# Performance work log

Hardware: AMD Instinct MI355X
Metric: run time of the kernel (lower is better)

The kernel has to match this reference:

```python
import jax, jax.numpy as jnp
import numpy as np

N_NODES = 50000
N_EDGES = 640000
D_IN = 128
D_OUT = 128


def setup_inputs() -> dict:
    key = jax.random.key(0)
    k1, k2, k3, k4, k5, k6 = jax.random.split(key, 6)
    nfeat = jax.random.normal(k1, (N_NODES, D_IN), dtype=jnp.float32)
    w = jax.random.uniform(k2, (N_EDGES,), dtype=jnp.float32)
    # nn.Linear weights are [out_feats, in_feats], Kaiming-uniform-ish scale
    bound = 1.0 / np.sqrt(D_IN)
    W1 = jax.random.uniform(k3, (D_OUT, D_IN), dtype=jnp.float32, minval=-bound, maxval=bound)
    W2 = jax.random.uniform(k4, (D_OUT, D_IN), dtype=jnp.float32, minval=-bound, maxval=bound)
    src = jax.random.randint(k5, (N_EDGES,), 0, N_NODES, dtype=jnp.int64)
    dst = jax.random.randint(k6, (N_EDGES,), 0, N_NODES, dtype=jnp.int64)
    return {"nfeat": nfeat, "w": w, "W1": W1, "W2": W2, "src": src, "dst": dst}


def reference(nfeat, w, W1, W2, src, dst):
    # feat_drop is identity in eval mode
    h = nfeat  # [N, D_IN]
    # update_all(u_mul_e('h','w','m'), sum('m','h_neighbor')):
    # gather source features, scale by per-edge scalar weight, scatter-sum to dst
    msg = h[src] * w[:, None]                                   # [E, D_IN]
    h_neighbor = jax.ops.segment_sum(msg, dst, num_segments=h.shape[0])  # [N, D_IN]
    # Bi-interaction residual: leaky_relu(Linear(h + hn)) + leaky_relu(Linear(h * hn))
    add_branch = jax.nn.leaky_relu((h + h_neighbor) @ W1.T, negative_slope=0.01)
    mul_branch = jax.nn.leaky_relu((h * h_neighbor) @ W2.T, negative_slope=0.01)
    out = add_branch + mul_branch                                # [N, D_OUT]
    return (h_neighbor, out)
```

## Files before the change

### kernel.cpp

```cpp
#include <hip/hip_runtime.h>
#include <hip/hip_bf16.h>

#define N_NODES 50000
#define N_EDGES 640000
#define D 128
#define OUT0_ELEMS (N_NODES * D)
#define SCAN_BLOCKS ((N_NODES + 255) / 256)

typedef __attribute__((ext_vector_type(8))) short short8v;
typedef __attribute__((ext_vector_type(4))) short short4v;
typedef __attribute__((ext_vector_type(4))) float f32x4;

static __device__ __forceinline__ unsigned short f2bf(float x) {
  __hip_bfloat16 b = __float2bfloat16(x);
  return *reinterpret_cast<unsigned short*>(&b);
}
static __device__ __forceinline__ float bf2f(unsigned short u) {
  unsigned x = ((unsigned)u) << 16;
  return __builtin_bit_cast(float, x);
}
static __device__ __forceinline__ unsigned pack_edge(int s, float wv) {
  return ((unsigned)f2bf(wv) << 16) | (unsigned)s;
}

__global__ __launch_bounds__(256) void conv_all(
    const float* __restrict__ nfeat, const float* __restrict__ W1,
    const float* __restrict__ W2, unsigned short* __restrict__ nf16,
    unsigned short* __restrict__ wc, int* __restrict__ cnt) {
  int i = blockIdx.x * 256 + threadIdx.x;
  int base = i * 8;
  float4 a = *(const float4*)(nfeat + base);
  float4 b = *(const float4*)(nfeat + base + 4);
  short8v o;
  o[0] = (short)f2bf(a.x); o[1] = (short)f2bf(a.y);
  o[2] = (short)f2bf(a.z); o[3] = (short)f2bf(a.w);
  o[4] = (short)f2bf(b.x); o[5] = (short)f2bf(b.y);
  o[6] = (short)f2bf(b.z); o[7] = (short)f2bf(b.w);
  *(short8v*)(nf16 + base) = o;
  if (i < D * D) {
    wc[i] = f2bf(W1[i]);
    wc[D * D + i] = f2bf(W2[i]);
  }
  if (i < N_NODES) cnt[i] = 0;
}

__global__ __launch_bounds__(256) void hist_rank(
    const int* __restrict__ dst, int* __restrict__ cnt, int* __restrict__ rank) {
  int t = blockIdx.x * 256 + threadIdx.x;
  int e = t * 4;
  if (e >= N_EDGES) return;
  int4 d4 = *(const int4*)(dst + e);
  int4 r4;
  r4.x = atomicAdd(&cnt[d4.x], 1);
  r4.y = atomicAdd(&cnt[d4.y], 1);
  r4.z = atomicAdd(&cnt[d4.z], 1);
  r4.w = atomicAdd(&cnt[d4.w], 1);
  *(int4*)(rank + e) = r4;
}

__global__ __launch_bounds__(256) void scan_block(
    const int* __restrict__ cnt, int* __restrict__ offs, int* __restrict__ bsums) {
  __shared__ int sdata[256];
  int t = threadIdx.x;
  int i = blockIdx.x * 256 + t;
  int v = (i < N_NODES) ? cnt[i] : 0;
  sdata[t] = v;
  __syncthreads();
#pragma unroll
  for (int off = 1; off < 256; off <<= 1) {
    int x = (t >= off) ? sdata[t - off] : 0;
    __syncthreads();
    sdata[t] += x;
    __syncthreads();
  }
  if (i < N_NODES) offs[i] = sdata[t] - v;
  if (t == 255) bsums[blockIdx.x] = sdata[t];
}

static __device__ __forceinline__ void scan_bsums_lds(
    const int* __restrict__ bsums, int* sincl) {
  int t = threadIdx.x;
  int v = (t < SCAN_BLOCKS) ? bsums[t] : 0;
  sincl[t] = v;
  __syncthreads();
#pragma unroll
  for (int off = 1; off < 256; off <<= 1) {
    int x = (t >= off) ? sincl[t - off] : 0;
    __syncthreads();
    sincl[t] += x;
    __syncthreads();
  }
}

__global__ __launch_bounds__(256) void fill4(
    const int* __restrict__ src, const int* __restrict__ dst,
    const float* __restrict__ w, const int* __restrict__ rank,
    const int* __restrict__ offs, const int* __restrict__ bsums,
    unsigned* __restrict__ es) {
  __shared__ int sincl[256];
  scan_bsums_lds(bsums, sincl);
  int t = blockIdx.x * 256 + threadIdx.x;
  int e = t * 4;
  if (e >= N_EDGES) return;
  int4 d4 = *(const int4*)(dst + e);
  int4 r4 = *(const int4*)(rank + e);
  int4 s4 = *(const int4*)(src + e);
  float4 w4 = *(const float4*)(w + e);
  int p0 = offs[d4.x] + ((d4.x >> 8) ? sincl[(d4.x >> 8) - 1] : 0) + r4.x;
  int p1 = offs[d4.y] + ((d4.y >> 8) ? sincl[(d4.y >> 8) - 1] : 0) + r4.y;
  int p2 = offs[d4.z] + ((d4.z >> 8) ? sincl[(d4.z >> 8) - 1] : 0) + r4.z;
  int p3 = offs[d4.w] + ((d4.w >> 8) ? sincl[(d4.w >> 8) - 1] : 0) + r4.w;
  es[p0] = pack_edge(s4.x, w4.x);
  es[p1] = pack_edge(s4.y, w4.y);
  es[p2] = pack_edge(s4.z, w4.z);
  es[p3] = pack_edge(s4.w, w4.w);
}

__global__ __launch_bounds__(256) void gather_bf16(
    const unsigned short* __restrict__ nf16, const int* __restrict__ offs,
    const int* __restrict__ bsums, const unsigned* __restrict__ es,
    float* __restrict__ hn) {
  __shared__ int sincl[256];
  scan_bsums_lds(bsums, sincl);

  int tid = blockIdx.x * 256 + threadIdx.x;
  int node = tid >> 4;
  if (node >= N_NODES) return;
  int q = tid & 15;

  int beg = offs[node] + ((node >> 8) ? sincl[(node >> 8) - 1] : 0);
  int end;
  {
    int n1 = node + 1;
    end = (n1 == N_NODES) ? N_EDGES
                          : offs[n1] + ((n1 >> 8) ? sincl[(n1 >> 8) - 1] : 0);
  }

  float acc[8];
#pragma unroll
  for (int j = 0; j < 8; ++j) acc[j] = 0.f;

  int k = beg;
  for (; k + 3 < end; k += 4) {
    unsigned r0 = es[k], r1 = es[k + 1], r2 = es[k + 2], r3 = es[k + 3];
    short8v v0 = *(const short8v*)(nf16 + (size_t)(r0 & 0xFFFF) * D + q * 8);
    short8v v1 = *(const short8v*)(nf16 + (size_t)(r1 & 0xFFFF) * D + q * 8);
    short8v v2 = *(const short8v*)(nf16 + (size_t)(r2 & 0xFFFF) * D + q * 8);
    short8v v3 = *(const short8v*)(nf16 + (size_t)(r3 & 0xFFFF) * D + q * 8);
    float w0 = bf2f((unsigned short)(r0 >> 16));
    float w1 = bf2f((unsigned short)(r1 >> 16));
    float w2 = bf2f((unsigned short)(r2 >> 16));
    float w3 = bf2f((unsigned short)(r3 >> 16));
#pragma unroll
    for (int j = 0; j < 8; ++j) {
      acc[j] += bf2f((unsigned short)v0[j]) * w0;
      acc[j] += bf2f((unsigned short)v1[j]) * w1;
      acc[j] += bf2f((unsigned short)v2[j]) * w2;
      acc[j] += bf2f((unsigned short)v3[j]) * w3;
    }
  }
  for (; k < end; ++k) {
    unsigned r0 = es[k];
    short8v v0 = *(const short8v*)(nf16 + (size_t)(r0 & 0xFFFF) * D + q * 8);
    float w0 = bf2f((unsigned short)(r0 >> 16));
#pragma unroll
    for (int j = 0; j < 8; ++j) acc[j] += bf2f((unsigned short)v0[j]) * w0;
  }

  float* orow = hn + (size_t)node * D + q * 8;
  *(float4*)(orow) = make_float4(acc[0], acc[1], acc[2], acc[3]);
  *(float4*)(orow + 4) = make_float4(acc[4], acc[5], acc[6], acc[7]);
}

__global__ __launch_bounds__(256) void bi_mfma_h16(
    const unsigned short* __restrict__ h16, const float* __restrict__ hn,
    const unsigned short* __restrict__ wc, float* __restrict__ out) {
  __shared__ __align__(16) unsigned short lds[2 * 64 * D];

  const int tid = threadIdx.x;
  const int lane = tid & 63;
  const int wid = tid >> 6;
  const int base = blockIdx.x * 64;
  const int r16 = lane & 15;
  const int kg = lane >> 4;

  short8v bf[2][2][4];
  {
    const int colbase = wid * 32;
#pragma unroll
    for (int g = 0; g < 2; ++g)
#pragma unroll
      for (int c = 0; c < 2; ++c)
#pragma unroll
        for (int ks = 0; ks < 4; ++ks) {
          int col = colbase + c * 16 + r16;
          int k = ks * 32 + kg * 8;
          bf[g][c][ks] =
              *(const short8v*)(wc + (size_t)g * D * D + (size_t)col * D + k);
        }
  }

#pragma unroll
  for (int p = 0; p < 8; ++p) {
    int flat = p * 1024 + tid * 4;
    int row = flat >> 7;
    int col = flat & 127;
    int node = base + row;
    float hx0 = 0.f, hx1 = 0.f, hx2 = 0.f, hx3 = 0.f;
    float4 nv = make_float4(0.f, 0.f, 0.f, 0.f);
    if (node < N_NODES) {
      short4v hv = *(const short4v*)(h16 + (size_t)node * D + col);
      hx0 = bf2f((unsigned short)hv[0]);
      hx1 = bf2f((unsigned short)hv[1]);
      hx2 = bf2f((unsigned short)hv[2]);
      hx3 = bf2f((unsigned short)hv[3]);
      nv = *(const float4*)(hn + (size_t)node * D + col);
    }
    short4v av, mv;
    av[0] = (short)f2bf(hx0 + nv.x);
    av[1] = (short)f2bf(hx1 + nv.y);
    av[2] = (short)f2bf(hx2 + nv.z);
    av[3] = (short)f2bf(hx3 + nv.w);
    mv[0] = (short)f2bf(hx0 * nv.x);
    mv[1] = (short)f2bf(hx1 * nv.y);
    mv[2] = (short)f2bf(hx2 * nv.z);
    mv[3] = (short)f2bf(hx3 * nv.w);
    int boff = (row * 256 + col * 2) ^ ((row & 7) << 4);
    *(short4v*)((char*)lds + boff) = av;
    *(short4v*)((char*)lds + 16384 + boff) = mv;
  }
  __syncthreads();

  f32x4 acc1[4][2], acc2[4][2];
#pragma unroll
  for (int rt = 0; rt < 4; ++rt)
#pragma unroll
    for (int c = 0; c < 2; ++c) {
      acc1[rt][c] = (f32x4){0.f, 0.f, 0.f, 0.f};
      acc2[rt][c] = (f32x4){0.f, 0.f, 0.f, 0.f};
    }

#pragma unroll
  for (int ks = 0; ks < 4; ++ks) {
#pragma unroll
    for (int rt = 0; rt < 4; ++rt) {
      int row = rt * 16 + r16;
      int boff = (row * 256 + (ks * 32 + kg * 8) * 2) ^ ((row & 7) << 4);
      short8v a1 = *(const short8v*)((const char*)lds + boff);
      short8v a2 = *(const short8v*)((const char*)lds + 16384 + boff);
#pragma unroll
      for (int c = 0; c < 2; ++c) {
        acc1[rt][c] = __builtin_amdgcn_mfma_f32_16x16x32_bf16(
            a1, bf[0][c][ks], acc1[rt][c], 0, 0, 0);
        acc2[rt][c] = __builtin_amdgcn_mfma_f32_16x16x32_bf16(
            a2, bf[1][c][ks], acc2[rt][c], 0, 0, 0);
      }
    }
  }

#pragma unroll
  for (int rt = 0; rt < 4; ++rt) {
#pragma unroll
    for (int c = 0; c < 2; ++c) {
#pragma unroll
      for (int e = 0; e < 4; ++e) {
        int row = rt * 16 + kg * 4 + e;
        int node = base + row;
        if (node < N_NODES) {
          int col = wid * 32 + c * 16 + r16;
          float x1 = acc1[rt][c][e];
          float x2 = acc2[rt][c][e];
          x1 = x1 > 0.f ? x1 : 0.01f * x1;
          x2 = x2 > 0.f ? x2 : 0.01f * x2;
          out[(size_t)node * D + col] = x1 + x2;
        }
      }
    }
  }
}

__global__ __launch_bounds__(256) void edge_scatter(
    const float* __restrict__ nfeat, const float* __restrict__ w,
    const int* __restrict__ src, const int* __restrict__ dst,
    float* __restrict__ hn) {
  int tid = blockIdx.x * 256 + threadIdx.x;
  int e = tid >> 5;
  if (e >= N_EDGES) return;
  int q = tid & 31;
  int s = src[e];
  int d = dst[e];
  float we = w[e];
  float4 v = ((const float4*)(nfeat + (size_t)s * D))[q];
  float* drow = hn + (size_t)d * D + q * 4;
  atomicAdd(drow + 0, v.x * we);
  atomicAdd(drow + 1, v.y * we);
  atomicAdd(drow + 2, v.z * we);
  atomicAdd(drow + 3, v.w * we);
}

__global__ __launch_bounds__(256) void bi_inter(
    const float* __restrict__ h, const float* __restrict__ hn,
    const float* __restrict__ W1, const float* __restrict__ W2,
    float* __restrict__ out) {
  int wid = __builtin_amdgcn_readfirstlane(threadIdx.x >> 6);
  int lane = threadIdx.x & 63;
  int node = blockIdx.x * 64 + lane;
  if (node >= N_NODES) return;
  const float4* h4 = (const float4*)(h + (size_t)node * D);
  const float4* n4 = (const float4*)(hn + (size_t)node * D);
  float acc1[32], acc2[32];
#pragma unroll
  for (int j = 0; j < 32; ++j) { acc1[j] = 0.f; acc2[j] = 0.f; }
  const int obase = wid * 32;
  for (int kq = 0; kq < 32; ++kq) {
    float4 hv = h4[kq];
    float4 nv = n4[kq];
    float a0 = hv.x + nv.x, a1 = hv.y + nv.y, a2 = hv.z + nv.z, a3 = hv.w + nv.w;
    float m0 = hv.x * nv.x, m1 = hv.y * nv.y, m2 = hv.z * nv.z, m3 = hv.w * nv.w;
#pragma unroll
    for (int j = 0; j < 32; ++j) {
      int o = obase + j;
      float4 w1 = *(const float4*)(W1 + (size_t)o * D + kq * 4);
      float4 w2 = *(const float4*)(W2 + (size_t)o * D + kq * 4);
      acc1[j] += a0 * w1.x + a1 * w1.y + a2 * w1.z + a3 * w1.w;
      acc2[j] += m0 * w2.x + m1 * w2.y + m2 * w2.z + m3 * w2.w;
    }
  }
  float* orow = out + (size_t)node * D + obase;
#pragma unroll
  for (int j = 0; j < 32; j += 4) {
    float4 r;
    float x;
    x = acc1[j + 0]; x = x > 0.f ? x : 0.01f * x;
    r.x = x; x = acc2[j + 0]; x = x > 0.f ? x : 0.01f * x; r.x += x;
    x = acc1[j + 1]; x = x > 0.f ? x : 0.01f * x;
    r.y = x; x = acc2[j + 1]; x = x > 0.f ? x : 0.01f * x; r.y += x;
    x = acc1[j + 2]; x = x > 0.f ? x : 0.01f * x;
    r.z = x; x = acc2[j + 2]; x = x > 0.f ? x : 0.01f * x; r.z += x;
    x = acc1[j + 3]; x = x > 0.f ? x : 0.01f * x;
    r.w = x; x = acc2[j + 3]; x = x > 0.f ? x : 0.01f * x; r.w += x;
    *(float4*)(orow + j) = r;
  }
}

extern "C" void kernel_launch(void* const* d_in, const int* in_sizes, int n_in,
                              void* d_out, int out_size, void* d_ws, size_t ws_size,
                              hipStream_t stream) {
  const float* nfeat = (const float*)d_in[0];
  const float* w     = (const float*)d_in[1];
  const float* W1    = (const float*)d_in[2];
  const float* W2    = (const float*)d_in[3];
  const int*   src   = (const int*)d_in[4];
  const int*   dst   = (const int*)d_in[5];

  float* hn  = (float*)d_out;
  float* out = (float*)d_out + OUT0_ELEMS;

  char* ws = (char*)d_ws;
  size_t off = 0;
  int* cnt = (int*)(ws + off);          off += (size_t)N_NODES * 4;
  int* offs = (int*)(ws + off);         off += (size_t)(N_NODES + 1) * 4;
  int* bsums = (int*)(ws + off);        off += 256 * 4;
  int* rank = (int*)(ws + off);         off += (size_t)N_EDGES * 4;
  unsigned* es = (unsigned*)(ws + off); off += (size_t)N_EDGES * 4;
  off = (off + 63) & ~(size_t)63;
  unsigned short* wc = (unsigned short*)(ws + off);
  off += (size_t)2 * D * D * 2;
  off = (off + 63) & ~(size_t)63;
  unsigned short* nf16 = (unsigned short*)(ws + off);
  off += (size_t)N_NODES * D * 2;
  size_t full_bytes = off;

  if (ws_size < full_bytes) {
    hipMemsetAsync(hn, 0, (size_t)OUT0_ELEMS * sizeof(float), stream);
    long long threads = (long long)N_EDGES * 32;
    int blocks = (int)((threads + 255) / 256);
    edge_scatter<<<blocks, 256, 0, stream>>>(nfeat, w, src, dst, hn);
    bi_inter<<<(N_NODES + 63) / 64, 256, 0, stream>>>(nfeat, hn, W1, W2, out);
    return;
  }

  conv_all<<<N_NODES * D / 8 / 256, 256, 0, stream>>>(
      nfeat, W1, W2, nf16, wc, cnt);
  hist_rank<<<N_EDGES / 4 / 256, 256, 0, stream>>>(dst, cnt, rank);
  scan_block<<<SCAN_BLOCKS, 256, 0, stream>>>(cnt, offs, bsums);
  fill4<<<N_EDGES / 4 / 256, 256, 0, stream>>>(src, dst, w, rank, offs,
                                               bsums, es);
  gather_bf16<<<(N_NODES * 16 + 255) / 256, 256, 0, stream>>>(
      nf16, offs, bsums, es, hn);
  bi_mfma_h16<<<(N_NODES + 63) / 64, 256, 0, stream>>>(nf16, hn, wc, out);
}
```

Measured before the change: 109.2 us.

## Gather neighbor features from column-chunked bf16 copy for cache locality

The conversion kernel now also writes the bf16 node features in a column-chunked layout: four chunks of 32 columns, each stored contiguously across all nodes. The gather kernel assigns each block one chunk and 64 nodes, with 4 threads per node. Each block's random row reads then touch only a 3.2 MB working set (64 bytes per node), which is meant to improve L2/MALL hit rates. In exchange it writes an extra 12.8 MB copy, reads the edge list four times, and issues more blocks.

```diff
diff --git a/kernel.cpp b/kernel.cpp
--- a/kernel.cpp
+++ b/kernel.cpp
@@ -7,6 +7,9 @@
 #define OUT0_ELEMS (N_NODES * D)
 #define SCAN_BLOCKS ((N_NODES + 255) / 256)
 
+#define GB_NODES 64
+#define GB_BLOCKS_PER_CHUNK ((N_NODES + GB_NODES - 1) / GB_NODES)
+
 typedef __attribute__((ext_vector_type(8))) short short8v;
 typedef __attribute__((ext_vector_type(4))) short short4v;
 typedef __attribute__((ext_vector_type(4))) float f32x4;
@@ -26,7 +29,8 @@
 __global__ __launch_bounds__(256) void conv_all(
     const float* __restrict__ nfeat, const float* __restrict__ W1,
     const float* __restrict__ W2, unsigned short* __restrict__ nf16,
-    unsigned short* __restrict__ wc, int* __restrict__ cnt) {
+    unsigned short* __restrict__ nf16t, unsigned short* __restrict__ wc,
+    int* __restrict__ cnt) {
   int i = blockIdx.x * 256 + threadIdx.x;
   int base = i * 8;
   float4 a = *(const float4*)(nfeat + base);
@@ -37,6 +41,13 @@
   o[4] = (short)f2bf(b.x); o[5] = (short)f2bf(b.y);
   o[6] = (short)f2bf(b.z); o[7] = (short)f2bf(b.w);
   *(short8v*)(nf16 + base) = o;
+  {
+    int node = base >> 7;
+    int col0 = base & 127;
+    int c = col0 >> 5;
+    int within = col0 & 31;
+    *(short8v*)(nf16t + ((size_t)c * N_NODES + node) * 32 + within) = o;
+  }
   if (i < D * D) {
     wc[i] = f2bf(W1[i]);
     wc[D * D + i] = f2bf(W2[i]);
@@ -116,17 +127,21 @@
   es[p3] = pack_edge(s4.w, w4.w);
 }
 
-__global__ __launch_bounds__(256) void gather_bf16(
-    const unsigned short* __restrict__ nf16, const int* __restrict__ offs,
+__global__ __launch_bounds__(256) void gather_chunk(
+    const unsigned short* __restrict__ nf16t, const int* __restrict__ offs,
     const int* __restrict__ bsums, const unsigned* __restrict__ es,
     float* __restrict__ hn) {
   __shared__ int sincl[256];
   scan_bsums_lds(bsums, sincl);
 
-  int tid = blockIdx.x * 256 + threadIdx.x;
-  int node = tid >> 4;
+  const int c = blockIdx.x & 3;
+  const int g = blockIdx.x >> 2;
+  const int tid = threadIdx.x;
+  const int node = g * GB_NODES + (tid >> 2);
   if (node >= N_NODES) return;
-  int q = tid & 15;
+  const int q = tid & 3;
+
+  const unsigned short* chunk = nf16t + (size_t)c * N_NODES * 32;
 
   int beg = offs[node] + ((node >> 8) ? sincl[(node >> 8) - 1] : 0);
   int end;
@@ -143,10 +158,10 @@
   int k = beg;
   for (; k + 3 < end; k += 4) {
     unsigned r0 = es[k], r1 = es[k + 1], r2 = es[k + 2], r3 = es[k + 3];
-    short8v v0 = *(const short8v*)(nf16 + (size_t)(r0 & 0xFFFF) * D + q * 8);
-    short8v v1 = *(const short8v*)(nf16 + (size_t)(r1 & 0xFFFF) * D + q * 8);
-    short8v v2 = *(const short8v*)(nf16 + (size_t)(r2 & 0xFFFF) * D + q * 8);
-    short8v v3 = *(const short8v*)(nf16 + (size_t)(r3 & 0xFFFF) * D + q * 8);
+    short8v v0 = *(const short8v*)(chunk + (size_t)(r0 & 0xFFFF) * 32 + q * 8);
+    short8v v1 = *(const short8v*)(chunk + (size_t)(r1 & 0xFFFF) * 32 + q * 8);
+    short8v v2 = *(const short8v*)(chunk + (size_t)(r2 & 0xFFFF) * 32 + q * 8);
+    short8v v3 = *(const short8v*)(chunk + (size_t)(r3 & 0xFFFF) * 32 + q * 8);
     float w0 = bf2f((unsigned short)(r0 >> 16));
     float w1 = bf2f((unsigned short)(r1 >> 16));
     float w2 = bf2f((unsigned short)(r2 >> 16));
@@ -161,13 +176,13 @@
   }
   for (; k < end; ++k) {
     unsigned r0 = es[k];
-    short8v v0 = *(const short8v*)(nf16 + (size_t)(r0 & 0xFFFF) * D + q * 8);
+    short8v v0 = *(const short8v*)(chunk + (size_t)(r0 & 0xFFFF) * 32 + q * 8);
     float w0 = bf2f((unsigned short)(r0 >> 16));
 #pragma unroll
     for (int j = 0; j < 8; ++j) acc[j] += bf2f((unsigned short)v0[j]) * w0;
   }
 
-  float* orow = hn + (size_t)node * D + q * 8;
+  float* orow = hn + (size_t)node * D + c * 32 + q * 8;
   *(float4*)(orow) = make_float4(acc[0], acc[1], acc[2], acc[3]);
   *(float4*)(orow + 4) = make_float4(acc[4], acc[5], acc[6], acc[7]);
 }
@@ -369,6 +384,9 @@
   off = (off + 63) & ~(size_t)63;
   unsigned short* nf16 = (unsigned short*)(ws + off);
   off += (size_t)N_NODES * D * 2;
+  off = (off + 63) & ~(size_t)63;
+  unsigned short* nf16t = (unsigned short*)(ws + off);
+  off += (size_t)N_NODES * D * 2;
   size_t full_bytes = off;
 
   if (ws_size < full_bytes) {
@@ -381,12 +399,12 @@
   }
 
   conv_all<<<N_NODES * D / 8 / 256, 256, 0, stream>>>(
-      nfeat, W1, W2, nf16, wc, cnt);
+      nfeat, W1, W2, nf16, nf16t, wc, cnt);
   hist_rank<<<N_EDGES / 4 / 256, 256, 0, stream>>>(dst, cnt, rank);
   scan_block<<<SCAN_BLOCKS, 256, 0, stream>>>(cnt, offs, bsums);
   fill4<<<N_EDGES / 4 / 256, 256, 0, stream>>>(src, dst, w, rank, offs,
                                                bsums, es);
-  gather_bf16<<<(N_NODES * 16 + 255) / 256, 256, 0, stream>>>(
-      nf16, offs, bsums, es, hn);
+  gather_chunk<<<4 * GB_BLOCKS_PER_CHUNK, 256, 0, stream>>>(
+      nf16t, offs, bsums, es, hn);
   bi_mfma_h16<<<(N_NODES + 63) / 64, 256, 0, stream>>>(nf16, hn, wc, out);
 }
```

Measured after the change: 105.1 us. 3.7% less time.
